# Kernel tuning notes

Measured on AMD Instinct MI355X. Metric: run time of the kernel, lower is better.

Reference implementation:

```python
import jax, jax.numpy as jnp
import numpy as np

EMBEDDING_DIM = 10
CONTEXT_SIZE_1 = 1
CONTEXT_SIZE_2 = 3
VOCAB = 50000
N = 1_000_000
NUM_NUMERIC = 16


def setup_inputs() -> dict:
    key = jax.random.key(0)
    ks = jax.random.split(key, 9)
    text_1 = jax.random.randint(ks[0], (N,), 0, VOCAB)
    text_2 = jax.random.randint(ks[1], (N,), 0, VOCAB)
    numeric_features = jax.random.normal(ks[2], (N, NUM_NUMERIC), dtype=jnp.float32)
    emb_table_1 = jax.random.normal(ks[3], (VOCAB, EMBEDDING_DIM), dtype=jnp.float32)
    emb_table_2 = jax.random.normal(ks[4], (VOCAB, EMBEDDING_DIM), dtype=jnp.float32)
    d_in = 2 * EMBEDDING_DIM + NUM_NUMERIC
    W1 = jax.random.normal(ks[5], (d_in, 128), dtype=jnp.float32) / np.sqrt(d_in)
    b1 = jnp.zeros((128,), dtype=jnp.float32)
    W2 = jax.random.normal(ks[6], (128, 1), dtype=jnp.float32) / np.sqrt(128.0)
    b2 = jnp.zeros((1,), dtype=jnp.float32)
    return {
        "text_1": text_1,
        "text_2": text_2,
        "numeric_features": numeric_features,
        "emb_table_1": emb_table_1,
        "emb_table_2": emb_table_2,
        "W1": W1,
        "b1": b1,
        "W2": W2,
        "b2": b2,
    }


def _contextual_embedding(ids, table, context_size):
    # mean of embeddings over window [i-cs, i+cs], clipped at sequence edges
    n = ids.shape[0]
    emb = table[ids]  # [N, D] gather
    # prefix sums with leading zero row: S[j] = sum(emb[0:j])
    S = jnp.concatenate([jnp.zeros((1, emb.shape[1]), emb.dtype),
                         jnp.cumsum(emb, axis=0)], axis=0)
    pos = jnp.arange(n)
    lo = jnp.maximum(pos - context_size, 0)
    hi = jnp.minimum(pos + context_size + 1, n)
    wsum = S[hi] - S[lo]                       # [N, D]
    count = (hi - lo).astype(emb.dtype)[:, None]
    return wsum / count


def reference(text_1, text_2, numeric_features, emb_table_1, emb_table_2, W1, b1, W2, b2):
    embed_1 = _contextual_embedding(text_1, emb_table_1, CONTEXT_SIZE_1)  # [N, 10]
    embed_2 = _contextual_embedding(text_2, emb_table_2, CONTEXT_SIZE_2)  # [N, 10]
    combined = jnp.concatenate([embed_1, embed_2, numeric_features], axis=1)
    h = jax.nn.relu(combined @ W1 + b1)
    out = h @ W2 + b2
    return jax.nn.sigmoid(out)  # [N, 1]
```

## Files before the change

kernel.cpp:

```cpp
#include <hip/hip_runtime.h>
#include <hip/hip_bf16.h>

#define EMB 10
#define DIN 36
#define HID 128
#define BM  128

typedef __attribute__((ext_vector_type(8))) short short8;
typedef __attribute__((ext_vector_type(4))) float f32x4;

union U8 { unsigned u[4]; short8 v; };

__device__ __forceinline__ short bf16_hi(float v) {
  __hip_bfloat16 h = __float2bfloat16(v);
  return *reinterpret_cast<short*>(&h);
}
__device__ __forceinline__ float bf16_to_f(short s) {
  __hip_bfloat16 h = *reinterpret_cast<__hip_bfloat16*>(&s);
  return __bfloat162float(h);
}

__device__ __forceinline__ void split_pair(float a, float b, unsigned &hi, unsigned &lo) {
  unsigned ua = __float_as_uint(a), ub = __float_as_uint(b);
  hi = __builtin_amdgcn_perm(ub, ua, 0x07060302u);
  float ra = a - __uint_as_float(ua & 0xFFFF0000u);
  float rb = b - __uint_as_float(ub & 0xFFFF0000u);
  lo = __builtin_amdgcn_perm(__float_as_uint(rb), __float_as_uint(ra), 0x07060302u);
}

__global__ void prep_kernel(const float* __restrict__ W1, const float* __restrict__ b1,
                            short* __restrict__ Bpack) {
  int b = blockIdx.x;
  int term = b >> 4;
  int ct   = (b >> 1) & 7;
  int ks   = b & 1;
  int l = threadIdx.x;
  int col = ct * 16 + (l & 15);
  int kb  = ks * 32 + (l >> 4) * 8;
  short8 o;
#pragma unroll
  for (int e = 0; e < 8; ++e) {
    int k = kb + e;
    float v = 0.0f;
    if (k < DIN)       v = W1[k * HID + col];
    else if (k == DIN) v = b1[col];
    short hb = bf16_hi(v);
    o[e] = (term == 0) ? hb : bf16_hi(v - bf16_to_f(hb));
  }
  *(short8*)(Bpack + (size_t)(((term * 8 + ct) * 2 + ks) * 64 + l) * 8) = o;
}

__global__ __launch_bounds__(256)
void fused_kernel(const int* __restrict__ t1, const int* __restrict__ t2,
                  const float* __restrict__ numf,
                  const float* __restrict__ tab1, const float* __restrict__ tab2,
                  const short* __restrict__ Bpack,
                  const float* __restrict__ W2, const float* __restrict__ b2,
                  float* __restrict__ out, int N) {
  __shared__ float E1[134][11];
  __shared__ float E2[136][11];
  __shared__ float Cs[BM][22];
  __shared__ float W2s[HID];

  const int tid = threadIdx.x;
  const long base = (long)blockIdx.x * BM;
  const int wid = tid >> 6;
  const int l = tid & 63;
  const int arow = l & 15;
  const int kg = l >> 4;

  const long rg0 = base + (long)(wid * 2) * 16 + arow;
  const long rg1 = rg0 + 16;
  float4 qa0 = {0,0,0,0}, qa1 = {0,0,0,0}, qb0 = {0,0,0,0}, qb1 = {0,0,0,0};
  if (kg == 0) {
    if (rg0 < (long)N) qa0 = *(const float4*)(numf + rg0 * 16 + 12);
    if (rg1 < (long)N) qa1 = *(const float4*)(numf + rg1 * 16 + 12);
  } else if (kg == 2) {
    if (rg0 < (long)N) qa0 = *(const float4*)(numf + rg0 * 16);
    if (rg1 < (long)N) qa1 = *(const float4*)(numf + rg1 * 16);
  } else if (kg == 3) {
    if (rg0 < (long)N) { qa0 = *(const float4*)(numf + rg0 * 16 + 4);
                         qb0 = *(const float4*)(numf + rg0 * 16 + 8); }
    if (rg1 < (long)N) { qa1 = *(const float4*)(numf + rg1 * 16 + 4);
                         qb1 = *(const float4*)(numf + rg1 * 16 + 8); }
  }

  if (tid < 130) {
    long g = base - 1 + tid;
    if (g >= 0 && g < (long)N) {
      const float2* src = (const float2*)(tab1 + (long)t1[g] * EMB);
#pragma unroll
      for (int i = 0; i < 5; ++i) {
        float2 v = src[i];
        E1[tid][2 * i] = v.x; E1[tid][2 * i + 1] = v.y;
      }
    } else {
#pragma unroll
      for (int i = 0; i < EMB; ++i) E1[tid][i] = 0.0f;
    }
  }
  {
    int h = tid - 122;
    if (h >= 0) {
      long g = base - 3 + h;
      if (g >= 0 && g < (long)N) {
        const float2* src = (const float2*)(tab2 + (long)t2[g] * EMB);
#pragma unroll
        for (int i = 0; i < 5; ++i) {
          float2 v = src[i];
          E2[h][2 * i] = v.x; E2[h][2 * i + 1] = v.y;
        }
      } else {
#pragma unroll
        for (int i = 0; i < EMB; ++i) E2[h][i] = 0.0f;
      }
    }
  }
  if (tid >= 128) W2s[tid - 128] = W2[tid - 128];
  __syncthreads();

  const bool edgeblk = (base == 0) || (base + BM + 3 > (long)N);
  if (tid < 120) {
    int grp = tid / 10, d = tid - grp * 10;
    int r0 = grp * 11;
    float e[13];
#pragma unroll
    for (int i = 0; i < 13; ++i) e[i] = E1[r0 + i][d];
    if (!edgeblk) {
#pragma unroll
      for (int i = 0; i < 11; ++i) {
        int rr = r0 + i;
        if (rr < BM) Cs[rr][d] = (e[i] + e[i + 1] + e[i + 2]) * (1.0f / 3.0f);
      }
    } else {
#pragma unroll
      for (int i = 0; i < 11; ++i) {
        int rr = r0 + i;
        if (rr < BM) {
          long row = base + rr;
          long lo = row - 1; if (lo < 0) lo = 0;
          long hi = row + 2; if (hi > (long)N) hi = (long)N;
          long c = hi - lo;  if (c < 1) c = 1;
          Cs[rr][d] = (e[i] + e[i + 1] + e[i + 2]) / (float)c;
        }
      }
    }
  } else if (tid < 250) {
    int u = tid - 120;
    int grp = u / 10, d = u - grp * 10;
    int r0 = grp * 10;
    float e[16];
#pragma unroll
    for (int i = 0; i < 16; ++i) e[i] = E2[r0 + i][d];
    float w = e[0] + e[1] + e[2] + e[3] + e[4] + e[5] + e[6];
    if (!edgeblk) {
#pragma unroll
      for (int i = 0; i < 10; ++i) {
        int rr = r0 + i;
        if (rr < BM) Cs[rr][10 + d] = w * (1.0f / 7.0f);
        if (i < 9) w += e[i + 7] - e[i];
      }
    } else {
#pragma unroll
      for (int i = 0; i < 10; ++i) {
        int rr = r0 + i;
        if (rr < BM) {
          long row = base + rr;
          long lo = row - 3; if (lo < 0) lo = 0;
          long hi = row + 4; if (hi > (long)N) hi = (long)N;
          long c = hi - lo;  if (c < 1) c = 1;
          Cs[rr][10 + d] = w / (float)c;
        }
        if (i < 9) w += e[i + 7] - e[i];
      }
    }
  }
  __syncthreads();

  short8 aHi[2][2], aLo[2][2];
#pragma unroll
  for (int rtl = 0; rtl < 2; ++rtl) {
    const int r = (wid * 2 + rtl) * 16 + arow;
    const float* crow = &Cs[r][0];
    const float4 qa = rtl ? qa1 : qa0;
    const float4 qb = rtl ? qb1 : qb0;
    U8 h0, l0, h1, l1;
    if (kg <= 1) {
#pragma unroll
      for (int i = 0; i < 4; ++i) {
        float2 t = *(const float2*)(crow + kg * 8 + 2 * i);
        split_pair(t.x, t.y, h0.u[i], l0.u[i]);
      }
    } else if (kg == 2) {
      float2 t0 = *(const float2*)(crow + 16);
      float2 t1 = *(const float2*)(crow + 18);
      split_pair(t0.x, t0.y, h0.u[0], l0.u[0]);
      split_pair(t1.x, t1.y, h0.u[1], l0.u[1]);
      split_pair(qa.x, qa.y, h0.u[2], l0.u[2]);
      split_pair(qa.z, qa.w, h0.u[3], l0.u[3]);
    } else {
      split_pair(qa.x, qa.y, h0.u[0], l0.u[0]);
      split_pair(qa.z, qa.w, h0.u[1], l0.u[1]);
      split_pair(qb.x, qb.y, h0.u[2], l0.u[2]);
      split_pair(qb.z, qb.w, h0.u[3], l0.u[3]);
    }
    if (kg == 0) {
      split_pair(qa.x, qa.y, h1.u[0], l1.u[0]);
      split_pair(qa.z, qa.w, h1.u[1], l1.u[1]);
      h1.u[2] = 0x00003F80u; l1.u[2] = 0u;
      h1.u[3] = 0u;          l1.u[3] = 0u;
    } else {
      h1.u[0] = h1.u[1] = h1.u[2] = h1.u[3] = 0u;
      l1.u[0] = l1.u[1] = l1.u[2] = l1.u[3] = 0u;
    }
    aHi[rtl][0] = h0.v; aLo[rtl][0] = l0.v;
    aHi[rtl][1] = h1.v; aLo[rtl][1] = l1.v;
  }

  float part[2][4] = {{0,0,0,0},{0,0,0,0}};
#pragma unroll
  for (int ct = 0; ct < 8; ++ct) {
    short8 bb[2][2];
#pragma unroll
    for (int term = 0; term < 2; ++term)
#pragma unroll
      for (int ks = 0; ks < 2; ++ks)
        bb[term][ks] = *(const short8*)(Bpack +
            (size_t)(((term * 8 + ct) * 2 + ks) * 64 + l) * 8);
    float w2c = W2s[ct * 16 + (l & 15)];
#pragma unroll
    for (int rtl = 0; rtl < 2; ++rtl) {
      f32x4 acc = {0.0f, 0.0f, 0.0f, 0.0f};
#pragma unroll
      for (int ks = 0; ks < 2; ++ks) {
        acc = __builtin_amdgcn_mfma_f32_16x16x32_bf16(aHi[rtl][ks], bb[0][ks], acc, 0, 0, 0);
        acc = __builtin_amdgcn_mfma_f32_16x16x32_bf16(aLo[rtl][ks], bb[0][ks], acc, 0, 0, 0);
        acc = __builtin_amdgcn_mfma_f32_16x16x32_bf16(aHi[rtl][ks], bb[1][ks], acc, 0, 0, 0);
      }
#pragma unroll
      for (int r = 0; r < 4; ++r) {
        float hv = fmaxf(acc[r], 0.0f);
        part[rtl][r] += hv * w2c;
      }
    }
  }
#pragma unroll
  for (int off = 1; off < 16; off <<= 1) {
#pragma unroll
    for (int rtl = 0; rtl < 2; ++rtl)
#pragma unroll
      for (int r = 0; r < 4; ++r)
        part[rtl][r] += __shfl_xor(part[rtl][r], off, 64);
  }
  if ((l & 15) < 4) {
    float b2v = b2[0];
#pragma unroll
    for (int rtl = 0; rtl < 2; ++rtl) {
      int rt = wid * 2 + rtl;
      long grow = base + rt * 16 + (l >> 4) * 4 + (l & 15);
      if (grow < (long)N) {
        float x = part[rtl][l & 15] + b2v;
        out[grow] = 1.0f / (1.0f + exp2f(x * -1.44269504f));
      }
    }
  }
}

extern "C" void kernel_launch(void* const* d_in, const int* in_sizes, int n_in,
                              void* d_out, int out_size, void* d_ws, size_t ws_size,
                              hipStream_t stream) {
  const int*   t1   = (const int*)d_in[0];
  const int*   t2   = (const int*)d_in[1];
  const float* numf = (const float*)d_in[2];
  const float* tab1 = (const float*)d_in[3];
  const float* tab2 = (const float*)d_in[4];
  const float* W1   = (const float*)d_in[5];
  const float* b1   = (const float*)d_in[6];
  const float* W2   = (const float*)d_in[7];
  const float* b2   = (const float*)d_in[8];
  float* out = (float*)d_out;
  const int N = in_sizes[0];
  short* Bpack = (short*)d_ws;

  hipLaunchKernelGGL(prep_kernel, dim3(32), dim3(64), 0, stream, W1, b1, Bpack);
  int nblk = (N + BM - 1) / BM;
  hipLaunchKernelGGL(fused_kernel, dim3(nblk), dim3(256), 0, stream,
                     t1, t2, numf, tab1, tab2, Bpack, W2, b2, out, N);
}
```

Baseline: 183.3 us.

## Make fused kernel persistent with register prefetch of next tile's gathers

The launch now uses a fixed grid of 1024 blocks, and each block loops over a contiguous range of 128-row tiles instead of running one block per tile. While the current tile computes, the next tile's index loads, embedding gathers and numeric features are prefetched into registers, hiding gather latency behind the MFMA work. Numeric features are now loaded coalesced and staged through shared memory, with Cs widened to 38 columns, which simplifies how the A fragments are assembled. The cost is extra register pressure and more LDS traffic. With only 1024 blocks, occupancy and latency hiding across blocks may also drop.

```diff
diff --git a/kernel.cpp b/kernel.cpp
--- a/kernel.cpp
+++ b/kernel.cpp
@@ -5,6 +5,7 @@
 #define DIN 36
 #define HID 128
 #define BM  128
+#define GRID 1024
 
 typedef __attribute__((ext_vector_type(8))) short short8;
 typedef __attribute__((ext_vector_type(4))) float f32x4;
@@ -56,211 +57,241 @@
                   const float* __restrict__ tab1, const float* __restrict__ tab2,
                   const short* __restrict__ Bpack,
                   const float* __restrict__ W2, const float* __restrict__ b2,
-                  float* __restrict__ out, int N) {
+                  float* __restrict__ out, int N, int ntiles) {
   __shared__ float E1[134][11];
   __shared__ float E2[136][11];
-  __shared__ float Cs[BM][22];
+  __shared__ float Cs[BM][38];
   __shared__ float W2s[HID];
 
   const int tid = threadIdx.x;
-  const long base = (long)blockIdx.x * BM;
-  const int wid = tid >> 6;
-  const int l = tid & 63;
-  const int arow = l & 15;
-  const int kg = l >> 4;
-
-  const long rg0 = base + (long)(wid * 2) * 16 + arow;
-  const long rg1 = rg0 + 16;
-  float4 qa0 = {0,0,0,0}, qa1 = {0,0,0,0}, qb0 = {0,0,0,0}, qb1 = {0,0,0,0};
-  if (kg == 0) {
-    if (rg0 < (long)N) qa0 = *(const float4*)(numf + rg0 * 16 + 12);
-    if (rg1 < (long)N) qa1 = *(const float4*)(numf + rg1 * 16 + 12);
-  } else if (kg == 2) {
-    if (rg0 < (long)N) qa0 = *(const float4*)(numf + rg0 * 16);
-    if (rg1 < (long)N) qa1 = *(const float4*)(numf + rg1 * 16);
-  } else if (kg == 3) {
-    if (rg0 < (long)N) { qa0 = *(const float4*)(numf + rg0 * 16 + 4);
-                         qb0 = *(const float4*)(numf + rg0 * 16 + 8); }
-    if (rg1 < (long)N) { qa1 = *(const float4*)(numf + rg1 * 16 + 4);
-                         qb1 = *(const float4*)(numf + rg1 * 16 + 8); }
+  const int wid = tid >> 6, l = tid & 63;
+  const int arow = l & 15, kg = l >> 4;
+  const int rloc = tid & 127, half = tid >> 7;
+  const int h2 = tid - 122;
+
+  const int G = GRID, bb_ = blockIdx.x;
+  const int q = ntiles / G, r = ntiles % G;
+  long tbeg, tend;
+  if (bb_ < r) { tbeg = (long)bb_ * (q + 1); tend = tbeg + q + 1; }
+  else         { tbeg = (long)r * (q + 1) + (long)(bb_ - r) * q; tend = tbeg + q; }
+
+  if (tid < HID) W2s[tid] = W2[tid];
+  const float b2v = b2[0];
+
+  long base = tbeg * BM;
+  float2 r1[5], r2[5];
+  float4 nfa = make_float4(0,0,0,0), nfb = make_float4(0,0,0,0);
+  {
+    int i1 = -1, i2 = -1;
+    if (tid < 130) { long g = base - 1 + tid; if (g >= 0 && g < (long)N) i1 = t1[g]; }
+    if (h2 >= 0)   { long g = base - 3 + h2;  if (g >= 0 && g < (long)N) i2 = t2[g]; }
+    if (i1 >= 0) {
+      const float2* s = (const float2*)(tab1 + (long)i1 * EMB);
+#pragma unroll
+      for (int i = 0; i < 5; ++i) r1[i] = s[i];
+    } else {
+#pragma unroll
+      for (int i = 0; i < 5; ++i) r1[i] = make_float2(0.f, 0.f);
+    }
+    if (i2 >= 0) {
+      const float2* s = (const float2*)(tab2 + (long)i2 * EMB);
+#pragma unroll
+      for (int i = 0; i < 5; ++i) r2[i] = s[i];
+    } else {
+#pragma unroll
+      for (int i = 0; i < 5; ++i) r2[i] = make_float2(0.f, 0.f);
+    }
+    long rowm = base + rloc;
+    if (rowm < (long)N) {
+      const float4* np = (const float4*)(numf + rowm * 16 + half * 8);
+      nfa = np[0]; nfb = np[1];
+    }
   }
 
-  if (tid < 130) {
-    long g = base - 1 + tid;
-    if (g >= 0 && g < (long)N) {
-      const float2* src = (const float2*)(tab1 + (long)t1[g] * EMB);
-#pragma unroll
-      for (int i = 0; i < 5; ++i) {
-        float2 v = src[i];
-        E1[tid][2 * i] = v.x; E1[tid][2 * i + 1] = v.y;
-      }
-    } else {
-#pragma unroll
-      for (int i = 0; i < EMB; ++i) E1[tid][i] = 0.0f;
-    }
-  }
-  {
-    int h = tid - 122;
-    if (h >= 0) {
-      long g = base - 3 + h;
-      if (g >= 0 && g < (long)N) {
-        const float2* src = (const float2*)(tab2 + (long)t2[g] * EMB);
-#pragma unroll
-        for (int i = 0; i < 5; ++i) {
-          float2 v = src[i];
-          E2[h][2 * i] = v.x; E2[h][2 * i + 1] = v.y;
+  for (long t = tbeg; t < tend; ++t) {
+    base = t * BM;
+    const long basen = base + BM;
+    const bool hasnext = (t + 1 < tend);
+
+    if (tid < 130) {
+#pragma unroll
+      for (int i = 0; i < 5; ++i) { E1[tid][2*i] = r1[i].x; E1[tid][2*i+1] = r1[i].y; }
+    }
+    if (h2 >= 0) {
+#pragma unroll
+      for (int i = 0; i < 5; ++i) { E2[h2][2*i] = r2[i].x; E2[h2][2*i+1] = r2[i].y; }
+    }
+    __syncthreads();
+
+    int i1n = -1, i2n = -1;
+    if (hasnext) {
+      if (tid < 130) { long g = basen - 1 + tid; if (g >= 0 && g < (long)N) i1n = t1[g]; }
+      if (h2 >= 0)   { long g = basen - 3 + h2;  if (g >= 0 && g < (long)N) i2n = t2[g]; }
+    }
+
+    const bool edgeblk = (base == 0) || (base + BM + 3 > (long)N);
+    if (tid < 120) {
+      int grp = tid / 10, d = tid - grp * 10;
+      int r0 = grp * 11;
+      float e[13];
+#pragma unroll
+      for (int i = 0; i < 13; ++i) e[i] = E1[r0 + i][d];
+      if (!edgeblk) {
+#pragma unroll
+        for (int i = 0; i < 11; ++i) {
+          int rr = r0 + i;
+          if (rr < BM) Cs[rr][d] = (e[i] + e[i + 1] + e[i + 2]) * (1.0f / 3.0f);
         }
       } else {
 #pragma unroll
-        for (int i = 0; i < EMB; ++i) E2[h][i] = 0.0f;
-      }
-    }
-  }
-  if (tid >= 128) W2s[tid - 128] = W2[tid - 128];
-  __syncthreads();
-
-  const bool edgeblk = (base == 0) || (base + BM + 3 > (long)N);
-  if (tid < 120) {
-    int grp = tid / 10, d = tid - grp * 10;
-    int r0 = grp * 11;
-    float e[13];
-#pragma unroll
-    for (int i = 0; i < 13; ++i) e[i] = E1[r0 + i][d];
-    if (!edgeblk) {
-#pragma unroll
-      for (int i = 0; i < 11; ++i) {
-        int rr = r0 + i;
-        if (rr < BM) Cs[rr][d] = (e[i] + e[i + 1] + e[i + 2]) * (1.0f / 3.0f);
-      }
-    } else {
-#pragma unroll
-      for (int i = 0; i < 11; ++i) {
-        int rr = r0 + i;
-        if (rr < BM) {
-          long row = base + rr;
-          long lo = row - 1; if (lo < 0) lo = 0;
-          long hi = row + 2; if (hi > (long)N) hi = (long)N;
-          long c = hi - lo;  if (c < 1) c = 1;
-          Cs[rr][d] = (e[i] + e[i + 1] + e[i + 2]) / (float)c;
-        }
-      }
-    }
-  } else if (tid < 250) {
-    int u = tid - 120;
-    int grp = u / 10, d = u - grp * 10;
-    int r0 = grp * 10;
-    float e[16];
-#pragma unroll
-    for (int i = 0; i < 16; ++i) e[i] = E2[r0 + i][d];
-    float w = e[0] + e[1] + e[2] + e[3] + e[4] + e[5] + e[6];
-    if (!edgeblk) {
-#pragma unroll
-      for (int i = 0; i < 10; ++i) {
-        int rr = r0 + i;
-        if (rr < BM) Cs[rr][10 + d] = w * (1.0f / 7.0f);
-        if (i < 9) w += e[i + 7] - e[i];
-      }
-    } else {
-#pragma unroll
-      for (int i = 0; i < 10; ++i) {
-        int rr = r0 + i;
-        if (rr < BM) {
-          long row = base + rr;
-          long lo = row - 3; if (lo < 0) lo = 0;
-          long hi = row + 4; if (hi > (long)N) hi = (long)N;
-          long c = hi - lo;  if (c < 1) c = 1;
-          Cs[rr][10 + d] = w / (float)c;
-        }
-        if (i < 9) w += e[i + 7] - e[i];
-      }
-    }
-  }
-  __syncthreads();
-
-  short8 aHi[2][2], aLo[2][2];
-#pragma unroll
-  for (int rtl = 0; rtl < 2; ++rtl) {
-    const int r = (wid * 2 + rtl) * 16 + arow;
-    const float* crow = &Cs[r][0];
-    const float4 qa = rtl ? qa1 : qa0;
-    const float4 qb = rtl ? qb1 : qb0;
-    U8 h0, l0, h1, l1;
-    if (kg <= 1) {
+        for (int i = 0; i < 11; ++i) {
+          int rr = r0 + i;
+          if (rr < BM) {
+            long row = base + rr;
+            long lo = row - 1; if (lo < 0) lo = 0;
+            long hi = row + 2; if (hi > (long)N) hi = (long)N;
+            long c = hi - lo;  if (c < 1) c = 1;
+            Cs[rr][d] = (e[i] + e[i + 1] + e[i + 2]) / (float)c;
+          }
+        }
+      }
+    } else if (tid < 250) {
+      int u = tid - 120;
+      int grp = u / 10, d = u - grp * 10;
+      int r0 = grp * 10;
+      float e[16];
+#pragma unroll
+      for (int i = 0; i < 16; ++i) e[i] = E2[r0 + i][d];
+      float w = e[0] + e[1] + e[2] + e[3] + e[4] + e[5] + e[6];
+      if (!edgeblk) {
+#pragma unroll
+        for (int i = 0; i < 10; ++i) {
+          int rr = r0 + i;
+          if (rr < BM) Cs[rr][10 + d] = w * (1.0f / 7.0f);
+          if (i < 9) w += e[i + 7] - e[i];
+        }
+      } else {
+#pragma unroll
+        for (int i = 0; i < 10; ++i) {
+          int rr = r0 + i;
+          if (rr < BM) {
+            long row = base + rr;
+            long lo = row - 3; if (lo < 0) lo = 0;
+            long hi = row + 4; if (hi > (long)N) hi = (long)N;
+            long c = hi - lo;  if (c < 1) c = 1;
+            Cs[rr][10 + d] = w / (float)c;
+          }
+          if (i < 9) w += e[i + 7] - e[i];
+        }
+      }
+    }
+    {
+      long rowm = base + rloc;
+      if (rowm < (long)N) {
+        float* cp = &Cs[rloc][20 + half * 8];
+        cp[0] = nfa.x; cp[1] = nfa.y; cp[2] = nfa.z; cp[3] = nfa.w;
+        cp[4] = nfb.x; cp[5] = nfb.y; cp[6] = nfb.z; cp[7] = nfb.w;
+      }
+      if (half == 0) { Cs[rloc][36] = 1.0f; Cs[rloc][37] = 0.0f; }
+    }
+    __syncthreads();
+
+    if (hasnext) {
+      if (tid < 130) {
+        if (i1n >= 0) {
+          const float2* s = (const float2*)(tab1 + (long)i1n * EMB);
+#pragma unroll
+          for (int i = 0; i < 5; ++i) r1[i] = s[i];
+        } else {
+#pragma unroll
+          for (int i = 0; i < 5; ++i) r1[i] = make_float2(0.f, 0.f);
+        }
+      }
+      if (h2 >= 0) {
+        if (i2n >= 0) {
+          const float2* s = (const float2*)(tab2 + (long)i2n * EMB);
+#pragma unroll
+          for (int i = 0; i < 5; ++i) r2[i] = s[i];
+        } else {
+#pragma unroll
+          for (int i = 0; i < 5; ++i) r2[i] = make_float2(0.f, 0.f);
+        }
+      }
+      long rowm = basen + rloc;
+      if (rowm < (long)N) {
+        const float4* np = (const float4*)(numf + rowm * 16 + half * 8);
+        nfa = np[0]; nfb = np[1];
+      } else { nfa = make_float4(0,0,0,0); nfb = make_float4(0,0,0,0); }
+    }
+
+    short8 aHi[2][2], aLo[2][2];
+#pragma unroll
+    for (int rtl = 0; rtl < 2; ++rtl) {
+      const int rr = (wid * 2 + rtl) * 16 + arow;
+      const float* crow = &Cs[rr][0];
+      U8 h0, l0, h1, l1;
 #pragma unroll
       for (int i = 0; i < 4; ++i) {
-        float2 t = *(const float2*)(crow + kg * 8 + 2 * i);
-        split_pair(t.x, t.y, h0.u[i], l0.u[i]);
-      }
-    } else if (kg == 2) {
-      float2 t0 = *(const float2*)(crow + 16);
-      float2 t1 = *(const float2*)(crow + 18);
-      split_pair(t0.x, t0.y, h0.u[0], l0.u[0]);
-      split_pair(t1.x, t1.y, h0.u[1], l0.u[1]);
-      split_pair(qa.x, qa.y, h0.u[2], l0.u[2]);
-      split_pair(qa.z, qa.w, h0.u[3], l0.u[3]);
-    } else {
-      split_pair(qa.x, qa.y, h0.u[0], l0.u[0]);
-      split_pair(qa.z, qa.w, h0.u[1], l0.u[1]);
-      split_pair(qb.x, qb.y, h0.u[2], l0.u[2]);
-      split_pair(qb.z, qb.w, h0.u[3], l0.u[3]);
-    }
-    if (kg == 0) {
-      split_pair(qa.x, qa.y, h1.u[0], l1.u[0]);
-      split_pair(qa.z, qa.w, h1.u[1], l1.u[1]);
-      h1.u[2] = 0x00003F80u; l1.u[2] = 0u;
-      h1.u[3] = 0u;          l1.u[3] = 0u;
-    } else {
-      h1.u[0] = h1.u[1] = h1.u[2] = h1.u[3] = 0u;
-      l1.u[0] = l1.u[1] = l1.u[2] = l1.u[3] = 0u;
-    }
-    aHi[rtl][0] = h0.v; aLo[rtl][0] = l0.v;
-    aHi[rtl][1] = h1.v; aLo[rtl][1] = l1.v;
-  }
-
-  float part[2][4] = {{0,0,0,0},{0,0,0,0}};
-#pragma unroll
-  for (int ct = 0; ct < 8; ++ct) {
-    short8 bb[2][2];
-#pragma unroll
-    for (int term = 0; term < 2; ++term)
-#pragma unroll
-      for (int ks = 0; ks < 2; ++ks)
-        bb[term][ks] = *(const short8*)(Bpack +
-            (size_t)(((term * 8 + ct) * 2 + ks) * 64 + l) * 8);
-    float w2c = W2s[ct * 16 + (l & 15)];
-#pragma unroll
-    for (int rtl = 0; rtl < 2; ++rtl) {
-      f32x4 acc = {0.0f, 0.0f, 0.0f, 0.0f};
-#pragma unroll
-      for (int ks = 0; ks < 2; ++ks) {
-        acc = __builtin_amdgcn_mfma_f32_16x16x32_bf16(aHi[rtl][ks], bb[0][ks], acc, 0, 0, 0);
-        acc = __builtin_amdgcn_mfma_f32_16x16x32_bf16(aLo[rtl][ks], bb[0][ks], acc, 0, 0, 0);
-        acc = __builtin_amdgcn_mfma_f32_16x16x32_bf16(aHi[rtl][ks], bb[1][ks], acc, 0, 0, 0);
-      }
-#pragma unroll
-      for (int r = 0; r < 4; ++r) {
-        float hv = fmaxf(acc[r], 0.0f);
-        part[rtl][r] += hv * w2c;
-      }
-    }
-  }
-#pragma unroll
-  for (int off = 1; off < 16; off <<= 1) {
-#pragma unroll
-    for (int rtl = 0; rtl < 2; ++rtl)
-#pragma unroll
-      for (int r = 0; r < 4; ++r)
-        part[rtl][r] += __shfl_xor(part[rtl][r], off, 64);
-  }
-  if ((l & 15) < 4) {
-    float b2v = b2[0];
-#pragma unroll
-    for (int rtl = 0; rtl < 2; ++rtl) {
-      int rt = wid * 2 + rtl;
-      long grow = base + rt * 16 + (l >> 4) * 4 + (l & 15);
-      if (grow < (long)N) {
-        float x = part[rtl][l & 15] + b2v;
-        out[grow] = 1.0f / (1.0f + exp2f(x * -1.44269504f));
+        float2 tt = *(const float2*)(crow + kg * 8 + 2 * i);
+        split_pair(tt.x, tt.y, h0.u[i], l0.u[i]);
+      }
+      if (kg == 0) {
+        float2 t0 = *(const float2*)(crow + 32);
+        float2 t1v = *(const float2*)(crow + 34);
+        float2 t2v = *(const float2*)(crow + 36);
+        split_pair(t0.x, t0.y, h1.u[0], l1.u[0]);
+        split_pair(t1v.x, t1v.y, h1.u[1], l1.u[1]);
+        split_pair(t2v.x, t2v.y, h1.u[2], l1.u[2]);
+        h1.u[3] = 0u; l1.u[3] = 0u;
+      } else {
+        h1.u[0] = h1.u[1] = h1.u[2] = h1.u[3] = 0u;
+        l1.u[0] = l1.u[1] = l1.u[2] = l1.u[3] = 0u;
+      }
+      aHi[rtl][0] = h0.v; aLo[rtl][0] = l0.v;
+      aHi[rtl][1] = h1.v; aLo[rtl][1] = l1.v;
+    }
+
+    float part[2][4] = {{0,0,0,0},{0,0,0,0}};
+#pragma unroll
+    for (int ct = 0; ct < 8; ++ct) {
+      short8 bh0 = *(const short8*)(Bpack + (size_t)(((0*8 + ct)*2 + 0)*64 + l)*8);
+      short8 bh1 = *(const short8*)(Bpack + (size_t)(((0*8 + ct)*2 + 1)*64 + l)*8);
+      short8 bl0 = *(const short8*)(Bpack + (size_t)(((1*8 + ct)*2 + 0)*64 + l)*8);
+      short8 bl1 = *(const short8*)(Bpack + (size_t)(((1*8 + ct)*2 + 1)*64 + l)*8);
+      float w2c = W2s[ct * 16 + (l & 15)];
+#pragma unroll
+      for (int rtl = 0; rtl < 2; ++rtl) {
+        f32x4 acc = {0.0f, 0.0f, 0.0f, 0.0f};
+        acc = __builtin_amdgcn_mfma_f32_16x16x32_bf16(aHi[rtl][0], bh0, acc, 0, 0, 0);
+        acc = __builtin_amdgcn_mfma_f32_16x16x32_bf16(aLo[rtl][0], bh0, acc, 0, 0, 0);
+        acc = __builtin_amdgcn_mfma_f32_16x16x32_bf16(aHi[rtl][0], bl0, acc, 0, 0, 0);
+        acc = __builtin_amdgcn_mfma_f32_16x16x32_bf16(aHi[rtl][1], bh1, acc, 0, 0, 0);
+        acc = __builtin_amdgcn_mfma_f32_16x16x32_bf16(aLo[rtl][1], bh1, acc, 0, 0, 0);
+        acc = __builtin_amdgcn_mfma_f32_16x16x32_bf16(aHi[rtl][1], bl1, acc, 0, 0, 0);
+#pragma unroll
+        for (int rg = 0; rg < 4; ++rg) {
+          float hv = fmaxf(acc[rg], 0.0f);
+          part[rtl][rg] += hv * w2c;
+        }
+      }
+    }
+#pragma unroll
+    for (int off = 1; off < 16; off <<= 1) {
+#pragma unroll
+      for (int rtl = 0; rtl < 2; ++rtl)
+#pragma unroll
+        for (int rg = 0; rg < 4; ++rg)
+          part[rtl][rg] += __shfl_xor(part[rtl][rg], off, 64);
+    }
+    if ((l & 15) < 4) {
+#pragma unroll
+      for (int rtl = 0; rtl < 2; ++rtl) {
+        int rt = wid * 2 + rtl;
+        long grow = base + rt * 16 + (l >> 4) * 4 + (l & 15);
+        if (grow < (long)N) {
+          float x = part[rtl][l & 15] + b2v;
+          out[grow] = 1.0f / (1.0f + exp2f(x * -1.44269504f));
+        }
       }
     }
   }
@@ -283,7 +314,7 @@
   short* Bpack = (short*)d_ws;
 
   hipLaunchKernelGGL(prep_kernel, dim3(32), dim3(64), 0, stream, W1, b1, Bpack);
-  int nblk = (N + BM - 1) / BM;
-  hipLaunchKernelGGL(fused_kernel, dim3(nblk), dim3(256), 0, stream,
-                     t1, t2, numf, tab1, tab2, Bpack, W2, b2, out, N);
-}
+  int ntiles = (N + BM - 1) / BM;
+  hipLaunchKernelGGL(fused_kernel, dim3(GRID), dim3(256), 0, stream,
+                     t1, t2, numf, tab1, tab2, Bpack, W2, b2, out, N, ntiles);
+}
```

Result: slower. 227.4 us (+24.1%).

## Compute window means directly in A-fragment build, drop Cs staging and second barrier

Applied to the files above, without the earlier changes.

Removes the intermediate shared Cs buffer and the separate window-mean pass. Each lane now sums the 3-row and 7-row windows straight from E1/E2 while building its MFMA A fragments, which eliminates one __syncthreads and a shared-memory write/read round trip. W2 is loaded into registers per lane instead of being staged through shared memory. The cost is redundant window summation across lanes, up to seven E2 row reads per lane, and a possibly worse LDS bank pattern now that the padding of 11 is gone.

```diff
diff --git a/kernel.cpp b/kernel.cpp
--- a/kernel.cpp
+++ b/kernel.cpp
@@ -57,17 +57,13 @@
                   const short* __restrict__ Bpack,
                   const float* __restrict__ W2, const float* __restrict__ b2,
                   float* __restrict__ out, int N) {
-  __shared__ float E1[134][11];
-  __shared__ float E2[136][11];
-  __shared__ float Cs[BM][22];
-  __shared__ float W2s[HID];
+  __shared__ float E1[130][10];
+  __shared__ float E2[134][10];
 
   const int tid = threadIdx.x;
   const long base = (long)blockIdx.x * BM;
-  const int wid = tid >> 6;
-  const int l = tid & 63;
-  const int arow = l & 15;
-  const int kg = l >> 4;
+  const int wid = tid >> 6, l = tid & 63;
+  const int arow = l & 15, kg = l >> 4;
 
   const long rg0 = base + (long)(wid * 2) * 16 + arow;
   const long rg1 = rg0 + 16;
@@ -84,6 +80,10 @@
     if (rg1 < (long)N) { qa1 = *(const float4*)(numf + rg1 * 16 + 4);
                          qb1 = *(const float4*)(numf + rg1 * 16 + 8); }
   }
+  float w2r[8];
+#pragma unroll
+  for (int ct = 0; ct < 8; ++ct) w2r[ct] = W2[ct * 16 + (l & 15)];
+  const float b2v = b2[0];
 
   if (tid < 130) {
     long g = base - 1 + tid;
@@ -100,102 +100,93 @@
     }
   }
   {
-    int h = tid - 122;
-    if (h >= 0) {
-      long g = base - 3 + h;
+    int h2 = tid - 122;
+    if (h2 >= 0) {
+      long g = base - 3 + h2;
       if (g >= 0 && g < (long)N) {
         const float2* src = (const float2*)(tab2 + (long)t2[g] * EMB);
 #pragma unroll
         for (int i = 0; i < 5; ++i) {
           float2 v = src[i];
-          E2[h][2 * i] = v.x; E2[h][2 * i + 1] = v.y;
+          E2[h2][2 * i] = v.x; E2[h2][2 * i + 1] = v.y;
         }
       } else {
 #pragma unroll
-        for (int i = 0; i < EMB; ++i) E2[h][i] = 0.0f;
-      }
-    }
-  }
-  if (tid >= 128) W2s[tid - 128] = W2[tid - 128];
+        for (int i = 0; i < EMB; ++i) E2[h2][i] = 0.0f;
+      }
+    }
+  }
   __syncthreads();
 
   const bool edgeblk = (base == 0) || (base + BM + 3 > (long)N);
-  if (tid < 120) {
-    int grp = tid / 10, d = tid - grp * 10;
-    int r0 = grp * 11;
-    float e[13];
-#pragma unroll
-    for (int i = 0; i < 13; ++i) e[i] = E1[r0 + i][d];
-    if (!edgeblk) {
-#pragma unroll
-      for (int i = 0; i < 11; ++i) {
-        int rr = r0 + i;
-        if (rr < BM) Cs[rr][d] = (e[i] + e[i + 1] + e[i + 2]) * (1.0f / 3.0f);
-      }
-    } else {
-#pragma unroll
-      for (int i = 0; i < 11; ++i) {
-        int rr = r0 + i;
-        if (rr < BM) {
-          long row = base + rr;
-          long lo = row - 1; if (lo < 0) lo = 0;
-          long hi = row + 2; if (hi > (long)N) hi = (long)N;
-          long c = hi - lo;  if (c < 1) c = 1;
-          Cs[rr][d] = (e[i] + e[i + 1] + e[i + 2]) / (float)c;
-        }
-      }
-    }
-  } else if (tid < 250) {
-    int u = tid - 120;
-    int grp = u / 10, d = u - grp * 10;
-    int r0 = grp * 10;
-    float e[16];
-#pragma unroll
-    for (int i = 0; i < 16; ++i) e[i] = E2[r0 + i][d];
-    float w = e[0] + e[1] + e[2] + e[3] + e[4] + e[5] + e[6];
-    if (!edgeblk) {
-#pragma unroll
-      for (int i = 0; i < 10; ++i) {
-        int rr = r0 + i;
-        if (rr < BM) Cs[rr][10 + d] = w * (1.0f / 7.0f);
-        if (i < 9) w += e[i + 7] - e[i];
-      }
-    } else {
-#pragma unroll
-      for (int i = 0; i < 10; ++i) {
-        int rr = r0 + i;
-        if (rr < BM) {
-          long row = base + rr;
-          long lo = row - 3; if (lo < 0) lo = 0;
-          long hi = row + 4; if (hi > (long)N) hi = (long)N;
-          long c = hi - lo;  if (c < 1) c = 1;
-          Cs[rr][10 + d] = w / (float)c;
-        }
-        if (i < 9) w += e[i + 7] - e[i];
-      }
-    }
-  }
-  __syncthreads();
-
   short8 aHi[2][2], aLo[2][2];
 #pragma unroll
   for (int rtl = 0; rtl < 2; ++rtl) {
-    const int r = (wid * 2 + rtl) * 16 + arow;
-    const float* crow = &Cs[r][0];
+    const int row0 = (wid * 2 + rtl) * 16 + arow;
+    const long g = base + row0;
     const float4 qa = rtl ? qa1 : qa0;
     const float4 qb = rtl ? qb1 : qb0;
+    float inv1 = (1.0f / 3.0f), inv2 = (1.0f / 7.0f);
+    if (edgeblk) {
+      long lo1 = g - 1; if (lo1 < 0) lo1 = 0;
+      long hi1 = g + 2; if (hi1 > (long)N) hi1 = (long)N;
+      long c1 = hi1 - lo1; if (c1 < 1) c1 = 1;
+      inv1 = 1.0f / (float)c1;
+      long lo2 = g - 3; if (lo2 < 0) lo2 = 0;
+      long hi2 = g + 4; if (hi2 > (long)N) hi2 = (long)N;
+      long c2 = hi2 - lo2; if (c2 < 1) c2 = 1;
+      inv2 = 1.0f / (float)c2;
+    }
     U8 h0, l0, h1, l1;
-    if (kg <= 1) {
-#pragma unroll
-      for (int i = 0; i < 4; ++i) {
-        float2 t = *(const float2*)(crow + kg * 8 + 2 * i);
-        split_pair(t.x, t.y, h0.u[i], l0.u[i]);
-      }
+    h1.u[0] = h1.u[1] = h1.u[2] = h1.u[3] = 0u;
+    l1.u[0] = l1.u[1] = l1.u[2] = l1.u[3] = 0u;
+    if (kg == 0) {
+      float v[8];
+#pragma unroll
+      for (int j = 0; j < 4; ++j) {
+        float2 x0 = *(const float2*)&E1[row0    ][2 * j];
+        float2 x1 = *(const float2*)&E1[row0 + 1][2 * j];
+        float2 x2 = *(const float2*)&E1[row0 + 2][2 * j];
+        v[2 * j]     = (x0.x + x1.x + x2.x) * inv1;
+        v[2 * j + 1] = (x0.y + x1.y + x2.y) * inv1;
+      }
+      split_pair(v[0], v[1], h0.u[0], l0.u[0]);
+      split_pair(v[2], v[3], h0.u[1], l0.u[1]);
+      split_pair(v[4], v[5], h0.u[2], l0.u[2]);
+      split_pair(v[6], v[7], h0.u[3], l0.u[3]);
+      split_pair(qa.x, qa.y, h1.u[0], l1.u[0]);
+      split_pair(qa.z, qa.w, h1.u[1], l1.u[1]);
+      h1.u[2] = 0x00003F80u;
+    } else if (kg == 1) {
+      float2 x0 = *(const float2*)&E1[row0    ][8];
+      float2 x1 = *(const float2*)&E1[row0 + 1][8];
+      float2 x2 = *(const float2*)&E1[row0 + 2][8];
+      float v0 = (x0.x + x1.x + x2.x) * inv1;
+      float v1 = (x0.y + x1.y + x2.y) * inv1;
+      float s0 = 0, s1 = 0, s2 = 0, s3 = 0, s4 = 0, s5 = 0;
+#pragma unroll
+      for (int dh = 0; dh < 7; ++dh) {
+        const float* er = &E2[row0 + dh][0];
+        float2 y0 = *(const float2*)(er + 0);
+        float2 y1 = *(const float2*)(er + 2);
+        float2 y2 = *(const float2*)(er + 4);
+        s0 += y0.x; s1 += y0.y; s2 += y1.x; s3 += y1.y; s4 += y2.x; s5 += y2.y;
+      }
+      split_pair(v0, v1, h0.u[0], l0.u[0]);
+      split_pair(s0 * inv2, s1 * inv2, h0.u[1], l0.u[1]);
+      split_pair(s2 * inv2, s3 * inv2, h0.u[2], l0.u[2]);
+      split_pair(s4 * inv2, s5 * inv2, h0.u[3], l0.u[3]);
     } else if (kg == 2) {
-      float2 t0 = *(const float2*)(crow + 16);
-      float2 t1 = *(const float2*)(crow + 18);
-      split_pair(t0.x, t0.y, h0.u[0], l0.u[0]);
-      split_pair(t1.x, t1.y, h0.u[1], l0.u[1]);
+      float s0 = 0, s1 = 0, s2 = 0, s3 = 0;
+#pragma unroll
+      for (int dh = 0; dh < 7; ++dh) {
+        const float* er = &E2[row0 + dh][6];
+        float2 y0 = *(const float2*)(er + 0);
+        float2 y1 = *(const float2*)(er + 2);
+        s0 += y0.x; s1 += y0.y; s2 += y1.x; s3 += y1.y;
+      }
+      split_pair(s0 * inv2, s1 * inv2, h0.u[0], l0.u[0]);
+      split_pair(s2 * inv2, s3 * inv2, h0.u[1], l0.u[1]);
       split_pair(qa.x, qa.y, h0.u[2], l0.u[2]);
       split_pair(qa.z, qa.w, h0.u[3], l0.u[3]);
     } else {
@@ -204,15 +195,6 @@
       split_pair(qb.x, qb.y, h0.u[2], l0.u[2]);
       split_pair(qb.z, qb.w, h0.u[3], l0.u[3]);
     }
-    if (kg == 0) {
-      split_pair(qa.x, qa.y, h1.u[0], l1.u[0]);
-      split_pair(qa.z, qa.w, h1.u[1], l1.u[1]);
-      h1.u[2] = 0x00003F80u; l1.u[2] = 0u;
-      h1.u[3] = 0u;          l1.u[3] = 0u;
-    } else {
-      h1.u[0] = h1.u[1] = h1.u[2] = h1.u[3] = 0u;
-      l1.u[0] = l1.u[1] = l1.u[2] = l1.u[3] = 0u;
-    }
     aHi[rtl][0] = h0.v; aLo[rtl][0] = l0.v;
     aHi[rtl][1] = h1.v; aLo[rtl][1] = l1.v;
   }
@@ -220,27 +202,24 @@
   float part[2][4] = {{0,0,0,0},{0,0,0,0}};
 #pragma unroll
   for (int ct = 0; ct < 8; ++ct) {
-    short8 bb[2][2];
-#pragma unroll
-    for (int term = 0; term < 2; ++term)
-#pragma unroll
-      for (int ks = 0; ks < 2; ++ks)
-        bb[term][ks] = *(const short8*)(Bpack +
-            (size_t)(((term * 8 + ct) * 2 + ks) * 64 + l) * 8);
-    float w2c = W2s[ct * 16 + (l & 15)];
+    short8 bh0 = *(const short8*)(Bpack + (size_t)(((0*8 + ct)*2 + 0)*64 + l)*8);
+    short8 bh1 = *(const short8*)(Bpack + (size_t)(((0*8 + ct)*2 + 1)*64 + l)*8);
+    short8 bl0 = *(const short8*)(Bpack + (size_t)(((1*8 + ct)*2 + 0)*64 + l)*8);
+    short8 bl1 = *(const short8*)(Bpack + (size_t)(((1*8 + ct)*2 + 1)*64 + l)*8);
+    float w2c = w2r[ct];
 #pragma unroll
     for (int rtl = 0; rtl < 2; ++rtl) {
       f32x4 acc = {0.0f, 0.0f, 0.0f, 0.0f};
-#pragma unroll
-      for (int ks = 0; ks < 2; ++ks) {
-        acc = __builtin_amdgcn_mfma_f32_16x16x32_bf16(aHi[rtl][ks], bb[0][ks], acc, 0, 0, 0);
-        acc = __builtin_amdgcn_mfma_f32_16x16x32_bf16(aLo[rtl][ks], bb[0][ks], acc, 0, 0, 0);
-        acc = __builtin_amdgcn_mfma_f32_16x16x32_bf16(aHi[rtl][ks], bb[1][ks], acc, 0, 0, 0);
-      }
-#pragma unroll
-      for (int r = 0; r < 4; ++r) {
-        float hv = fmaxf(acc[r], 0.0f);
-        part[rtl][r] += hv * w2c;
+      acc = __builtin_amdgcn_mfma_f32_16x16x32_bf16(aHi[rtl][0], bh0, acc, 0, 0, 0);
+      acc = __builtin_amdgcn_mfma_f32_16x16x32_bf16(aLo[rtl][0], bh0, acc, 0, 0, 0);
+      acc = __builtin_amdgcn_mfma_f32_16x16x32_bf16(aHi[rtl][0], bl0, acc, 0, 0, 0);
+      acc = __builtin_amdgcn_mfma_f32_16x16x32_bf16(aHi[rtl][1], bh1, acc, 0, 0, 0);
+      acc = __builtin_amdgcn_mfma_f32_16x16x32_bf16(aLo[rtl][1], bh1, acc, 0, 0, 0);
+      acc = __builtin_amdgcn_mfma_f32_16x16x32_bf16(aHi[rtl][1], bl1, acc, 0, 0, 0);
+#pragma unroll
+      for (int rg = 0; rg < 4; ++rg) {
+        float hv = fmaxf(acc[rg], 0.0f);
+        part[rtl][rg] += hv * w2c;
       }
     }
   }
@@ -249,11 +228,10 @@
 #pragma unroll
     for (int rtl = 0; rtl < 2; ++rtl)
 #pragma unroll
-      for (int r = 0; r < 4; ++r)
-        part[rtl][r] += __shfl_xor(part[rtl][r], off, 64);
+      for (int rg = 0; rg < 4; ++rg)
+        part[rtl][rg] += __shfl_xor(part[rtl][rg], off, 64);
   }
   if ((l & 15) < 4) {
-    float b2v = b2[0];
 #pragma unroll
     for (int rtl = 0; rtl < 2; ++rtl) {
       int rt = wid * 2 + rtl;
```

Measured after the change: 258.0 us. 1.41x slower.

## Make fused kernel persistent with LDS-resident packed weights and register W2

Applied to the files above, without the earlier changes.

Launches a fixed grid of 1024 blocks that each loop over a contiguous range of 128-row tiles, instead of one block per tile. The packed bf16 W1 split (32 KB) is copied once per block into shared memory and W2 is held in registers, so the weights are no longer re-read from global memory for every tile. The cost is more LDS per block (lower occupancy) and no overlap between one tile's gathers and its compute, since each tile still syncs twice.

```diff
diff --git a/kernel.cpp b/kernel.cpp
--- a/kernel.cpp
+++ b/kernel.cpp
@@ -5,6 +5,7 @@
 #define DIN 36
 #define HID 128
 #define BM  128
+#define GRID 1024
 
 typedef __attribute__((ext_vector_type(8))) short short8;
 typedef __attribute__((ext_vector_type(4))) float f32x4;
@@ -56,211 +57,221 @@
                   const float* __restrict__ tab1, const float* __restrict__ tab2,
                   const short* __restrict__ Bpack,
                   const float* __restrict__ W2, const float* __restrict__ b2,
-                  float* __restrict__ out, int N) {
+                  float* __restrict__ out, int N, int ntiles) {
   __shared__ float E1[134][11];
   __shared__ float E2[136][11];
   __shared__ float Cs[BM][22];
-  __shared__ float W2s[HID];
+  __shared__ short Bs[16384];
 
   const int tid = threadIdx.x;
-  const long base = (long)blockIdx.x * BM;
-  const int wid = tid >> 6;
-  const int l = tid & 63;
-  const int arow = l & 15;
-  const int kg = l >> 4;
-
-  const long rg0 = base + (long)(wid * 2) * 16 + arow;
-  const long rg1 = rg0 + 16;
-  float4 qa0 = {0,0,0,0}, qa1 = {0,0,0,0}, qb0 = {0,0,0,0}, qb1 = {0,0,0,0};
-  if (kg == 0) {
-    if (rg0 < (long)N) qa0 = *(const float4*)(numf + rg0 * 16 + 12);
-    if (rg1 < (long)N) qa1 = *(const float4*)(numf + rg1 * 16 + 12);
-  } else if (kg == 2) {
-    if (rg0 < (long)N) qa0 = *(const float4*)(numf + rg0 * 16);
-    if (rg1 < (long)N) qa1 = *(const float4*)(numf + rg1 * 16);
-  } else if (kg == 3) {
-    if (rg0 < (long)N) { qa0 = *(const float4*)(numf + rg0 * 16 + 4);
-                         qb0 = *(const float4*)(numf + rg0 * 16 + 8); }
-    if (rg1 < (long)N) { qa1 = *(const float4*)(numf + rg1 * 16 + 4);
-                         qb1 = *(const float4*)(numf + rg1 * 16 + 8); }
+  const int wid = tid >> 6, l = tid & 63;
+  const int arow = l & 15, kg = l >> 4;
+  const int h2 = tid - 122;
+
+  {
+    const float4* src = (const float4*)Bpack;
+    float4* dst = (float4*)Bs;
+#pragma unroll
+    for (int i = 0; i < 8; ++i) dst[tid + 256 * i] = src[tid + 256 * i];
   }
-
-  if (tid < 130) {
-    long g = base - 1 + tid;
-    if (g >= 0 && g < (long)N) {
-      const float2* src = (const float2*)(tab1 + (long)t1[g] * EMB);
-#pragma unroll
-      for (int i = 0; i < 5; ++i) {
-        float2 v = src[i];
-        E1[tid][2 * i] = v.x; E1[tid][2 * i + 1] = v.y;
-      }
-    } else {
-#pragma unroll
-      for (int i = 0; i < EMB; ++i) E1[tid][i] = 0.0f;
-    }
-  }
-  {
-    int h = tid - 122;
-    if (h >= 0) {
-      long g = base - 3 + h;
+  float w2r[8];
+#pragma unroll
+  for (int ct = 0; ct < 8; ++ct) w2r[ct] = W2[ct * 16 + (l & 15)];
+  const float b2v = b2[0];
+
+  const int q = ntiles / GRID, r = ntiles % GRID;
+  int tbeg, tend;
+  if ((int)blockIdx.x < r) { tbeg = blockIdx.x * (q + 1); tend = tbeg + q + 1; }
+  else { tbeg = r * (q + 1) + ((int)blockIdx.x - r) * q; tend = tbeg + q; }
+
+  for (int t = tbeg; t < tend; ++t) {
+    const long base = (long)t * BM;
+
+    const long rg0 = base + (long)(wid * 2) * 16 + arow;
+    const long rg1 = rg0 + 16;
+    float4 qa0 = {0,0,0,0}, qa1 = {0,0,0,0}, qb0 = {0,0,0,0}, qb1 = {0,0,0,0};
+    if (kg == 0) {
+      if (rg0 < (long)N) qa0 = *(const float4*)(numf + rg0 * 16 + 12);
+      if (rg1 < (long)N) qa1 = *(const float4*)(numf + rg1 * 16 + 12);
+    } else if (kg == 2) {
+      if (rg0 < (long)N) qa0 = *(const float4*)(numf + rg0 * 16);
+      if (rg1 < (long)N) qa1 = *(const float4*)(numf + rg1 * 16);
+    } else if (kg == 3) {
+      if (rg0 < (long)N) { qa0 = *(const float4*)(numf + rg0 * 16 + 4);
+                           qb0 = *(const float4*)(numf + rg0 * 16 + 8); }
+      if (rg1 < (long)N) { qa1 = *(const float4*)(numf + rg1 * 16 + 4);
+                           qb1 = *(const float4*)(numf + rg1 * 16 + 8); }
+    }
+
+    if (tid < 130) {
+      long g = base - 1 + tid;
+      if (g >= 0 && g < (long)N) {
+        const float2* src = (const float2*)(tab1 + (long)t1[g] * EMB);
+#pragma unroll
+        for (int i = 0; i < 5; ++i) {
+          float2 v = src[i];
+          E1[tid][2 * i] = v.x; E1[tid][2 * i + 1] = v.y;
+        }
+      } else {
+#pragma unroll
+        for (int i = 0; i < EMB; ++i) E1[tid][i] = 0.0f;
+      }
+    }
+    if (h2 >= 0) {
+      long g = base - 3 + h2;
       if (g >= 0 && g < (long)N) {
         const float2* src = (const float2*)(tab2 + (long)t2[g] * EMB);
 #pragma unroll
         for (int i = 0; i < 5; ++i) {
           float2 v = src[i];
-          E2[h][2 * i] = v.x; E2[h][2 * i + 1] = v.y;
-        }
-      } else {
-#pragma unroll
-        for (int i = 0; i < EMB; ++i) E2[h][i] = 0.0f;
-      }
-    }
-  }
-  if (tid >= 128) W2s[tid - 128] = W2[tid - 128];
-  __syncthreads();
-
-  const bool edgeblk = (base == 0) || (base + BM + 3 > (long)N);
-  if (tid < 120) {
-    int grp = tid / 10, d = tid - grp * 10;
-    int r0 = grp * 11;
-    float e[13];
-#pragma unroll
-    for (int i = 0; i < 13; ++i) e[i] = E1[r0 + i][d];
-    if (!edgeblk) {
-#pragma unroll
-      for (int i = 0; i < 11; ++i) {
-        int rr = r0 + i;
-        if (rr < BM) Cs[rr][d] = (e[i] + e[i + 1] + e[i + 2]) * (1.0f / 3.0f);
-      }
-    } else {
-#pragma unroll
-      for (int i = 0; i < 11; ++i) {
-        int rr = r0 + i;
-        if (rr < BM) {
-          long row = base + rr;
-          long lo = row - 1; if (lo < 0) lo = 0;
-          long hi = row + 2; if (hi > (long)N) hi = (long)N;
-          long c = hi - lo;  if (c < 1) c = 1;
-          Cs[rr][d] = (e[i] + e[i + 1] + e[i + 2]) / (float)c;
-        }
-      }
-    }
-  } else if (tid < 250) {
-    int u = tid - 120;
-    int grp = u / 10, d = u - grp * 10;
-    int r0 = grp * 10;
-    float e[16];
-#pragma unroll
-    for (int i = 0; i < 16; ++i) e[i] = E2[r0 + i][d];
-    float w = e[0] + e[1] + e[2] + e[3] + e[4] + e[5] + e[6];
-    if (!edgeblk) {
-#pragma unroll
-      for (int i = 0; i < 10; ++i) {
-        int rr = r0 + i;
-        if (rr < BM) Cs[rr][10 + d] = w * (1.0f / 7.0f);
-        if (i < 9) w += e[i + 7] - e[i];
-      }
-    } else {
-#pragma unroll
-      for (int i = 0; i < 10; ++i) {
-        int rr = r0 + i;
-        if (rr < BM) {
-          long row = base + rr;
-          long lo = row - 3; if (lo < 0) lo = 0;
-          long hi = row + 4; if (hi > (long)N) hi = (long)N;
-          long c = hi - lo;  if (c < 1) c = 1;
-          Cs[rr][10 + d] = w / (float)c;
-        }
-        if (i < 9) w += e[i + 7] - e[i];
-      }
-    }
-  }
-  __syncthreads();
-
-  short8 aHi[2][2], aLo[2][2];
-#pragma unroll
-  for (int rtl = 0; rtl < 2; ++rtl) {
-    const int r = (wid * 2 + rtl) * 16 + arow;
-    const float* crow = &Cs[r][0];
-    const float4 qa = rtl ? qa1 : qa0;
-    const float4 qb = rtl ? qb1 : qb0;
-    U8 h0, l0, h1, l1;
-    if (kg <= 1) {
-#pragma unroll
-      for (int i = 0; i < 4; ++i) {
-        float2 t = *(const float2*)(crow + kg * 8 + 2 * i);
-        split_pair(t.x, t.y, h0.u[i], l0.u[i]);
-      }
-    } else if (kg == 2) {
-      float2 t0 = *(const float2*)(crow + 16);
-      float2 t1 = *(const float2*)(crow + 18);
-      split_pair(t0.x, t0.y, h0.u[0], l0.u[0]);
-      split_pair(t1.x, t1.y, h0.u[1], l0.u[1]);
-      split_pair(qa.x, qa.y, h0.u[2], l0.u[2]);
-      split_pair(qa.z, qa.w, h0.u[3], l0.u[3]);
-    } else {
-      split_pair(qa.x, qa.y, h0.u[0], l0.u[0]);
-      split_pair(qa.z, qa.w, h0.u[1], l0.u[1]);
-      split_pair(qb.x, qb.y, h0.u[2], l0.u[2]);
-      split_pair(qb.z, qb.w, h0.u[3], l0.u[3]);
-    }
-    if (kg == 0) {
-      split_pair(qa.x, qa.y, h1.u[0], l1.u[0]);
-      split_pair(qa.z, qa.w, h1.u[1], l1.u[1]);
-      h1.u[2] = 0x00003F80u; l1.u[2] = 0u;
-      h1.u[3] = 0u;          l1.u[3] = 0u;
-    } else {
-      h1.u[0] = h1.u[1] = h1.u[2] = h1.u[3] = 0u;
-      l1.u[0] = l1.u[1] = l1.u[2] = l1.u[3] = 0u;
-    }
-    aHi[rtl][0] = h0.v; aLo[rtl][0] = l0.v;
-    aHi[rtl][1] = h1.v; aLo[rtl][1] = l1.v;
-  }
-
-  float part[2][4] = {{0,0,0,0},{0,0,0,0}};
-#pragma unroll
-  for (int ct = 0; ct < 8; ++ct) {
-    short8 bb[2][2];
-#pragma unroll
-    for (int term = 0; term < 2; ++term)
-#pragma unroll
-      for (int ks = 0; ks < 2; ++ks)
-        bb[term][ks] = *(const short8*)(Bpack +
-            (size_t)(((term * 8 + ct) * 2 + ks) * 64 + l) * 8);
-    float w2c = W2s[ct * 16 + (l & 15)];
+          E2[h2][2 * i] = v.x; E2[h2][2 * i + 1] = v.y;
+        }
+      } else {
+#pragma unroll
+        for (int i = 0; i < EMB; ++i) E2[h2][i] = 0.0f;
+      }
+    }
+    __syncthreads();
+
+    const bool edgeblk = (base == 0) || (base + BM + 3 > (long)N);
+    if (tid < 120) {
+      int grp = tid / 10, d = tid - grp * 10;
+      int r0 = grp * 11;
+      float e[13];
+#pragma unroll
+      for (int i = 0; i < 13; ++i) e[i] = E1[r0 + i][d];
+      if (!edgeblk) {
+#pragma unroll
+        for (int i = 0; i < 11; ++i) {
+          int rr = r0 + i;
+          if (rr < BM) Cs[rr][d] = (e[i] + e[i + 1] + e[i + 2]) * (1.0f / 3.0f);
+        }
+      } else {
+#pragma unroll
+        for (int i = 0; i < 11; ++i) {
+          int rr = r0 + i;
+          if (rr < BM) {
+            long row = base + rr;
+            long lo = row - 1; if (lo < 0) lo = 0;
+            long hi = row + 2; if (hi > (long)N) hi = (long)N;
+            long c = hi - lo;  if (c < 1) c = 1;
+            Cs[rr][d] = (e[i] + e[i + 1] + e[i + 2]) / (float)c;
+          }
+        }
+      }
+    } else if (tid < 250) {
+      int u = tid - 120;
+      int grp = u / 10, d = u - grp * 10;
+      int r0 = grp * 10;
+      float e[16];
+#pragma unroll
+      for (int i = 0; i < 16; ++i) e[i] = E2[r0 + i][d];
+      float w = e[0] + e[1] + e[2] + e[3] + e[4] + e[5] + e[6];
+      if (!edgeblk) {
+#pragma unroll
+        for (int i = 0; i < 10; ++i) {
+          int rr = r0 + i;
+          if (rr < BM) Cs[rr][10 + d] = w * (1.0f / 7.0f);
+          if (i < 9) w += e[i + 7] - e[i];
+        }
+      } else {
+#pragma unroll
+        for (int i = 0; i < 10; ++i) {
+          int rr = r0 + i;
+          if (rr < BM) {
+            long row = base + rr;
+            long lo = row - 3; if (lo < 0) lo = 0;
+            long hi = row + 4; if (hi > (long)N) hi = (long)N;
+            long c = hi - lo;  if (c < 1) c = 1;
+            Cs[rr][10 + d] = w / (float)c;
+          }
+          if (i < 9) w += e[i + 7] - e[i];
+        }
+      }
+    }
+    __syncthreads();
+
+    short8 aHi[2][2], aLo[2][2];
 #pragma unroll
     for (int rtl = 0; rtl < 2; ++rtl) {
-      f32x4 acc = {0.0f, 0.0f, 0.0f, 0.0f};
-#pragma unroll
-      for (int ks = 0; ks < 2; ++ks) {
-        acc = __builtin_amdgcn_mfma_f32_16x16x32_bf16(aHi[rtl][ks], bb[0][ks], acc, 0, 0, 0);
-        acc = __builtin_amdgcn_mfma_f32_16x16x32_bf16(aLo[rtl][ks], bb[0][ks], acc, 0, 0, 0);
-        acc = __builtin_amdgcn_mfma_f32_16x16x32_bf16(aHi[rtl][ks], bb[1][ks], acc, 0, 0, 0);
-      }
-#pragma unroll
-      for (int r = 0; r < 4; ++r) {
-        float hv = fmaxf(acc[r], 0.0f);
-        part[rtl][r] += hv * w2c;
-      }
-    }
-  }
-#pragma unroll
-  for (int off = 1; off < 16; off <<= 1) {
-#pragma unroll
-    for (int rtl = 0; rtl < 2; ++rtl)
-#pragma unroll
-      for (int r = 0; r < 4; ++r)
-        part[rtl][r] += __shfl_xor(part[rtl][r], off, 64);
-  }
-  if ((l & 15) < 4) {
-    float b2v = b2[0];
-#pragma unroll
-    for (int rtl = 0; rtl < 2; ++rtl) {
-      int rt = wid * 2 + rtl;
-      long grow = base + rt * 16 + (l >> 4) * 4 + (l & 15);
-      if (grow < (long)N) {
-        float x = part[rtl][l & 15] + b2v;
-        out[grow] = 1.0f / (1.0f + exp2f(x * -1.44269504f));
+      const int rr = (wid * 2 + rtl) * 16 + arow;
+      const float* crow = &Cs[rr][0];
+      const float4 qa = rtl ? qa1 : qa0;
+      const float4 qb = rtl ? qb1 : qb0;
+      U8 h0, l0, h1, l1;
+      if (kg <= 1) {
+#pragma unroll
+        for (int i = 0; i < 4; ++i) {
+          float2 tt = *(const float2*)(crow + kg * 8 + 2 * i);
+          split_pair(tt.x, tt.y, h0.u[i], l0.u[i]);
+        }
+      } else if (kg == 2) {
+        float2 t0 = *(const float2*)(crow + 16);
+        float2 t1v = *(const float2*)(crow + 18);
+        split_pair(t0.x, t0.y, h0.u[0], l0.u[0]);
+        split_pair(t1v.x, t1v.y, h0.u[1], l0.u[1]);
+        split_pair(qa.x, qa.y, h0.u[2], l0.u[2]);
+        split_pair(qa.z, qa.w, h0.u[3], l0.u[3]);
+      } else {
+        split_pair(qa.x, qa.y, h0.u[0], l0.u[0]);
+        split_pair(qa.z, qa.w, h0.u[1], l0.u[1]);
+        split_pair(qb.x, qb.y, h0.u[2], l0.u[2]);
+        split_pair(qb.z, qb.w, h0.u[3], l0.u[3]);
+      }
+      if (kg == 0) {
+        split_pair(qa.x, qa.y, h1.u[0], l1.u[0]);
+        split_pair(qa.z, qa.w, h1.u[1], l1.u[1]);
+        h1.u[2] = 0x00003F80u; l1.u[2] = 0u;
+        h1.u[3] = 0u;          l1.u[3] = 0u;
+      } else {
+        h1.u[0] = h1.u[1] = h1.u[2] = h1.u[3] = 0u;
+        l1.u[0] = l1.u[1] = l1.u[2] = l1.u[3] = 0u;
+      }
+      aHi[rtl][0] = h0.v; aLo[rtl][0] = l0.v;
+      aHi[rtl][1] = h1.v; aLo[rtl][1] = l1.v;
+    }
+
+    float part[2][4] = {{0,0,0,0},{0,0,0,0}};
+#pragma unroll
+    for (int ct = 0; ct < 8; ++ct) {
+      short8 bh0 = *(const short8*)&Bs[(size_t)(((0*8 + ct)*2 + 0)*64 + l) * 8];
+      short8 bh1 = *(const short8*)&Bs[(size_t)(((0*8 + ct)*2 + 1)*64 + l) * 8];
+      short8 bl0 = *(const short8*)&Bs[(size_t)(((1*8 + ct)*2 + 0)*64 + l) * 8];
+      short8 bl1 = *(const short8*)&Bs[(size_t)(((1*8 + ct)*2 + 1)*64 + l) * 8];
+      float w2c = w2r[ct];
+#pragma unroll
+      for (int rtl = 0; rtl < 2; ++rtl) {
+        f32x4 acc = {0.0f, 0.0f, 0.0f, 0.0f};
+        acc = __builtin_amdgcn_mfma_f32_16x16x32_bf16(aHi[rtl][0], bh0, acc, 0, 0, 0);
+        acc = __builtin_amdgcn_mfma_f32_16x16x32_bf16(aLo[rtl][0], bh0, acc, 0, 0, 0);
+        acc = __builtin_amdgcn_mfma_f32_16x16x32_bf16(aHi[rtl][0], bl0, acc, 0, 0, 0);
+        acc = __builtin_amdgcn_mfma_f32_16x16x32_bf16(aHi[rtl][1], bh1, acc, 0, 0, 0);
+        acc = __builtin_amdgcn_mfma_f32_16x16x32_bf16(aLo[rtl][1], bh1, acc, 0, 0, 0);
+        acc = __builtin_amdgcn_mfma_f32_16x16x32_bf16(aHi[rtl][1], bl1, acc, 0, 0, 0);
+#pragma unroll
+        for (int rg = 0; rg < 4; ++rg) {
+          float hv = fmaxf(acc[rg], 0.0f);
+          part[rtl][rg] += hv * w2c;
+        }
+      }
+    }
+#pragma unroll
+    for (int off = 1; off < 16; off <<= 1) {
+#pragma unroll
+      for (int rtl = 0; rtl < 2; ++rtl)
+#pragma unroll
+        for (int rg = 0; rg < 4; ++rg)
+          part[rtl][rg] += __shfl_xor(part[rtl][rg], off, 64);
+    }
+    if ((l & 15) < 4) {
+#pragma unroll
+      for (int rtl = 0; rtl < 2; ++rtl) {
+        int rt = wid * 2 + rtl;
+        long grow = base + rt * 16 + (l >> 4) * 4 + (l & 15);
+        if (grow < (long)N) {
+          float x = part[rtl][l & 15] + b2v;
+          out[grow] = 1.0f / (1.0f + exp2f(x * -1.44269504f));
+        }
       }
     }
   }
@@ -283,7 +294,7 @@
   short* Bpack = (short*)d_ws;
 
   hipLaunchKernelGGL(prep_kernel, dim3(32), dim3(64), 0, stream, W1, b1, Bpack);
-  int nblk = (N + BM - 1) / BM;
-  hipLaunchKernelGGL(fused_kernel, dim3(nblk), dim3(256), 0, stream,
-                     t1, t2, numf, tab1, tab2, Bpack, W2, b2, out, N);
-}
+  int ntiles = (N + BM - 1) / BM;
+  hipLaunchKernelGGL(fused_kernel, dim3(GRID), dim3(256), 0, stream,
+                     t1, t2, numf, tab1, tab2, Bpack, W2, b2, out, N, ntiles);
+}
```

Result: slower. 208.8 us (+13.9%).
